# Kernel tuning notes

Measured on AMD Instinct MI355X. Metric: run time of the kernel, lower is better.

## Reference

```python
import jax, jax.numpy as jnp
import numpy as np

IN_DIM = 128
OUT_DIM = 128
HEADS = 4
HEAD_DIM = OUT_DIM // HEADS
N_NODES = 50000
N_EDGES = 800000
NEG_SLOPE = 0.2
LN_EPS = 1e-5


def setup_inputs() -> dict:
    key = jax.random.key(0)
    ks = jax.random.split(key, 10)
    x = jax.random.normal(ks[0], (N_NODES, IN_DIM), dtype=jnp.float32)
    edge_index = jax.random.randint(ks[1], (2, N_EDGES), 0, N_NODES, dtype=jnp.int64)
    s = 1.0 / np.sqrt(IN_DIM)
    W_l = jax.random.normal(ks[2], (IN_DIM, HEADS * HEAD_DIM), dtype=jnp.float32) * s
    b_l = jnp.zeros((HEADS * HEAD_DIM,), dtype=jnp.float32)
    W_r = jax.random.normal(ks[3], (IN_DIM, HEADS * HEAD_DIM), dtype=jnp.float32) * s
    b_r = jnp.zeros((HEADS * HEAD_DIM,), dtype=jnp.float32)
    att = jax.random.normal(ks[4], (HEADS, HEAD_DIM), dtype=jnp.float32) * (1.0 / np.sqrt(HEAD_DIM))
    bias = jnp.zeros((HEADS * HEAD_DIM,), dtype=jnp.float32)
    gamma = jnp.ones((OUT_DIM,), dtype=jnp.float32)
    beta = jnp.zeros((OUT_DIM,), dtype=jnp.float32)
    return {"x": x, "edge_index": edge_index, "W_l": W_l, "b_l": b_l,
            "W_r": W_r, "b_r": b_r, "att": att, "bias": bias,
            "gamma": gamma, "beta": beta}


def reference(x, edge_index, W_l, b_l, W_r, b_r, att, bias, gamma, beta):
    N = x.shape[0]
    src, dst = edge_index[0], edge_index[1]
    # GATv2: separate linear transforms for source and target nodes
    xl = (x @ W_l + b_l).reshape(N, HEADS, HEAD_DIM)  # source / message features
    xr = (x @ W_r + b_r).reshape(N, HEADS, HEAD_DIM)  # target features
    # per-edge attention logits: a^T . leaky_relu(xl[src] + xr[dst])  -> [E, H]
    h = jax.nn.leaky_relu(xl[src] + xr[dst], NEG_SLOPE)
    e = jnp.einsum('ehd,hd->eh', h, att)
    # segment softmax over edges grouped by destination node
    m = jax.ops.segment_max(e, dst, num_segments=N)
    m = jnp.where(jnp.isfinite(m), m, 0.0)  # guard empty segments
    ex = jnp.exp(e - m[dst])
    denom = jax.ops.segment_sum(ex, dst, num_segments=N)
    alpha = ex / (denom[dst] + 1e-16)  # [E, H]
    # scatter-add weighted source features (dropout omitted: eval mode)
    out = jax.ops.segment_sum(alpha[:, :, None] * xl[src], dst, num_segments=N)
    out = out.reshape(N, HEADS * HEAD_DIM) + bias
    # residual (in_dim == out_dim) + LayerNorm
    out = out + x
    mu = out.mean(axis=-1, keepdims=True)
    var = ((out - mu) ** 2).mean(axis=-1, keepdims=True)
    return (out - mu) * jax.lax.rsqrt(var + LN_EPS) * gamma + beta
```

## Files before the change

kernel.cpp:

```cpp
#include <hip/hip_runtime.h>
#include <math.h>

#define NEG_SLOPE 0.2f
#define LN_EPS 1e-5f
#define CAP 64
#define HB 4096
#define RUN 56
#define XSTR 136
#define SMEM_BYTES (64 * XSTR * 2)

typedef __attribute__((ext_vector_type(8))) short s8v;
typedef __attribute__((ext_vector_type(8))) unsigned short u8v;
typedef __attribute__((ext_vector_type(4))) float f4v;
typedef _Float16 h2 __attribute__((ext_vector_type(2)));

__device__ inline unsigned short f2bf(float f) {
    unsigned u = __float_as_uint(f);
    return (unsigned short)((u + 0x7FFFu + ((u >> 16) & 1u)) >> 16);
}

__global__ __launch_bounds__(256) void pre_scat_kernel(
    const int* __restrict__ src, const int* __restrict__ dst,
    const float* __restrict__ Wl, const float* __restrict__ Wr,
    unsigned short* __restrict__ packL, unsigned short* __restrict__ packR,
    unsigned* __restrict__ part, int* __restrict__ cntmat,
    int E, int NBKT) {
    const int bid = blockIdx.x, tid = threadIdx.x;
    if (bid < 2) {
        const float* W = bid ? Wr : Wl;
        unsigned short* pk = bid ? packR : packL;
        #pragma unroll
        for (int it = 0; it < 16; ++it) {
            int pos4 = tid + it * 256;
            int k = pos4 >> 5, c4 = pos4 & 31;
            float4 v = *(const float4*)&W[k * 128 + c4 * 4];
            int t = k >> 5, lane_hi = (k & 31) >> 3, j = k & 7;
            float vv[4] = {v.x, v.y, v.z, v.w};
            #pragma unroll
            for (int u = 0; u < 4; ++u) {
                int n = c4 * 4 + u;
                int idx = ((((n >> 4) * 4 + t) * 64) + lane_hi * 16 + (n & 15)) * 8 + j;
                pk[idx] = f2bf(vv[u]);
            }
        }
        return;
    }
    __shared__ int cnt[256];
    const int sb = bid - 2;
    const int e0 = sb * HB;
    cnt[tid] = 0;
    __syncthreads();
    for (int j = tid; j < HB; j += 256) {
        int e = e0 + j;
        if (e < E) {
            int d = dst[e];
            int b = d >> 8;
            int r = atomicAdd(&cnt[b], 1);
            if (r < RUN)
                part[((size_t)sb * NBKT + b) * RUN + r] =
                    ((unsigned)(d & 255) << 16) | (unsigned)src[e];
        }
    }
    __syncthreads();
    if (tid < NBKT) {
        int c = cnt[tid]; if (c > RUN) c = RUN;
        cntmat[(size_t)sb * NBKT + tid] = c;
    }
}

__global__ __launch_bounds__(256, 4) void fill_tf_kernel(
    const unsigned* __restrict__ part, const int* __restrict__ cntmat,
    unsigned short* __restrict__ csr, int* __restrict__ deg,
    const float* __restrict__ x,
    const unsigned short* __restrict__ packL, const unsigned short* __restrict__ packR,
    const float* __restrict__ bl, const float* __restrict__ br,
    _Float16* __restrict__ xl, _Float16* __restrict__ xr,
    int N, int NBKT, int NSC) {
    const int bid = blockIdx.x, tid = threadIdx.x;
    __shared__ __align__(16) char smem[SMEM_BYTES];

    if (bid < NBKT) {
        int* cur = (int*)smem;
        cur[tid] = 0;
        __syncthreads();
        const int b = bid;
        if (tid < NSC) {
            int cnt = cntmat[(size_t)tid * NBKT + b];
            const unsigned* seg = part + ((size_t)tid * NBKT + b) * RUN;
            for (int i = 0; i < cnt; ++i) {
                unsigned rec = seg[i];
                int dl = rec >> 16;
                int pos = atomicAdd(&cur[dl], 1);
                if (pos < CAP)
                    csr[(size_t)(b * 256 + dl) * CAP + (((pos & 3) << 4) | (pos >> 2))] =
                        (unsigned short)(rec & 0xFFFFu);
            }
        }
        __syncthreads();
        int node = b * 256 + tid;
        if (node < N) deg[node] = cur[tid];
        return;
    }

    unsigned short* xs = (unsigned short*)smem;
    const int tb = bid - NBKT;
    const int blk0 = tb * 64;

    #pragma unroll
    for (int it = 0; it < 8; ++it) {
        int slot = tid + it * 256;
        int row = slot >> 5, c4 = slot & 31;
        int node = blk0 + row;
        float4 v = make_float4(0.f, 0.f, 0.f, 0.f);
        if (node < N) v = *(const float4*)&x[(size_t)node * 128 + 4 * c4];
        ushort4 o;
        o.x = f2bf(v.x); o.y = f2bf(v.y); o.z = f2bf(v.z); o.w = f2bf(v.w);
        *(ushort4*)&xs[row * XSTR + 4 * c4] = o;
    }
    __syncthreads();

    const int wv = tid >> 6, lane = tid & 63;
    const int row = lane & 15, q = lane >> 4;
    const int node0 = blk0 + wv * 16;

    s8v afrag[4];
    #pragma unroll
    for (int t = 0; t < 4; ++t)
        afrag[t] = *(const s8v*)&xs[(wv * 16 + row) * XSTR + t * 32 + q * 8];

    #pragma unroll 1
    for (int side = 0; side < 2; ++side) {
        const unsigned short* __restrict__ pk = side ? packR : packL;
        const float* __restrict__ bb = side ? br : bl;
        _Float16* __restrict__ dsth = side ? xr : xl;

        f4v acc[8];
        #pragma unroll
        for (int nt = 0; nt < 8; ++nt) acc[nt] = (f4v){0.f, 0.f, 0.f, 0.f};

        #pragma unroll
        for (int t = 0; t < 4; ++t) {
            #pragma unroll
            for (int np = 0; np < 2; ++np) {
                s8v bfr[4];
                #pragma unroll
                for (int u = 0; u < 4; ++u)
                    bfr[u] = *(const s8v*)&pk[(((np * 4 + u) * 4 + t) * 64 + lane) * 8];
                #pragma unroll
                for (int u = 0; u < 4; ++u)
                    acc[np * 4 + u] = __builtin_amdgcn_mfma_f32_16x16x32_bf16(
                        afrag[t], bfr[u], acc[np * 4 + u], 0, 0, 0);
            }
        }

        #pragma unroll
        for (int nt = 0; nt < 8; ++nt) {
            float bcol = bb[nt * 16 + row];
            #pragma unroll
            for (int r2 = 0; r2 < 4; ++r2) {
                int nd = node0 + q * 4 + r2;
                if (nd < N)
                    dsth[(size_t)nd * 128 + nt * 16 + row] = (_Float16)(acc[nt][r2] + bcol);
            }
        }
    }
}

__device__ inline void edge_body(float4 raw, const h2* xr2, const h2* av2,
                                 h2 ns2, float& den, float* acc) {
    h2 c[4];
    c[0] = __builtin_bit_cast(h2, raw.x);
    c[1] = __builtin_bit_cast(h2, raw.y);
    c[2] = __builtin_bit_cast(h2, raw.z);
    c[3] = __builtin_bit_cast(h2, raw.w);
    float p = 0.f;
    #pragma unroll
    for (int j = 0; j < 4; ++j) {
        h2 t = c[j] + xr2[j];
        h2 hh = __builtin_elementwise_max(t, t * ns2);
#if __has_builtin(__builtin_amdgcn_fdot2)
        p = __builtin_amdgcn_fdot2(hh, av2[j], p, false);
#else
        p = fmaf((float)hh.x, (float)av2[j].x, p);
        p = fmaf((float)hh.y, (float)av2[j].y, p);
#endif
    }
    p += __shfl_xor(p, 1);
    p += __shfl_xor(p, 2);
    float w = __expf(p);
    den += w;
    #pragma unroll
    for (int j = 0; j < 4; ++j) {
        acc[2 * j]     = fmaf(w, (float)c[j].x, acc[2 * j]);
        acc[2 * j + 1] = fmaf(w, (float)c[j].y, acc[2 * j + 1]);
    }
}

__global__ __launch_bounds__(256) void gat_kernel(
    const int* __restrict__ deg_arr, const unsigned short* __restrict__ csr,
    const _Float16* __restrict__ xl, const _Float16* __restrict__ xr,
    const float* __restrict__ att, const float* __restrict__ x,
    const float* __restrict__ bias, const float* __restrict__ gamma,
    const float* __restrict__ beta, float* __restrict__ out, int N) {
    const int node = blockIdx.x * 4 + (threadIdx.x >> 6);
    const int lane = threadIdx.x & 63;
    if (node >= N) return;
    const int sub = lane & 15;
    const int eg  = lane >> 4;
    const int f0  = sub * 8;

    int dg = deg_arr[node]; if (dg > CAP) dg = CAP;
    const unsigned short* crow = csr + (size_t)node * CAP;
    u8v cidx = *(const u8v*)&crow[eg * 16];

    h2 xr2[4], av2[4];
    {
        float4 xrw = *(const float4*)&xr[(size_t)node * 128 + f0];
        float fw[4]; fw[0] = xrw.x; fw[1] = xrw.y; fw[2] = xrw.z; fw[3] = xrw.w;
        #pragma unroll
        for (int j = 0; j < 4; ++j) xr2[j] = __builtin_bit_cast(h2, fw[j]);
        float4 c0 = *(const float4*)&att[f0];
        float4 c1 = *(const float4*)&att[f0 + 4];
        av2[0] = (h2){(_Float16)c0.x, (_Float16)c0.y};
        av2[1] = (h2){(_Float16)c0.z, (_Float16)c0.w};
        av2[2] = (h2){(_Float16)c1.x, (_Float16)c1.y};
        av2[3] = (h2){(_Float16)c1.z, (_Float16)c1.w};
    }
    const h2 ns2 = (h2){(_Float16)NEG_SLOPE, (_Float16)NEG_SLOPE};

    float4 bufv[8];
    #pragma unroll
    for (int k = 0; k < 8; ++k) {
        int i = eg + 4 * k;
        if (i < dg) bufv[k] = *(const float4*)&xl[(size_t)(unsigned short)cidx[k] * 128 + f0];
    }

    float den0 = 0.f, den1 = 0.f;
    float a0[8] = {0,0,0,0,0,0,0,0}, a1[8] = {0,0,0,0,0,0,0,0};

    #pragma unroll
    for (int k = 0; k < 8; k += 2) {
        if (eg + 4 * k < dg)       edge_body(bufv[k],     xr2, av2, ns2, den0, a0);
        if (eg + 4 * (k + 1) < dg) edge_body(bufv[k + 1], xr2, av2, ns2, den1, a1);
    }

    if (dg > 32) {
        u8v cidx2 = *(const u8v*)&crow[eg * 16 + 8];
        #pragma unroll
        for (int k = 0; k < 8; ++k) {
            int i = eg + 32 + 4 * k;
            if (i < dg) {
                float4 raw = *(const float4*)&xl[(size_t)(unsigned short)cidx2[k] * 128 + f0];
                edge_body(raw, xr2, av2, ns2, (k & 1) ? den1 : den0, (k & 1) ? a1 : a0);
            }
        }
    }

    float den = den0 + den1;
    float acc[8];
    #pragma unroll
    for (int j = 0; j < 8; ++j) acc[j] = a0[j] + a1[j];

    den += __shfl_xor(den, 16); den += __shfl_xor(den, 32);
    #pragma unroll
    for (int j = 0; j < 8; ++j) {
        acc[j] += __shfl_xor(acc[j], 16);
        acc[j] += __shfl_xor(acc[j], 32);
    }

    const float inv = 1.0f / (den + 1e-16f);
    float v[8];
    {
        float4 b0 = *(const float4*)&bias[f0];
        float4 b1 = *(const float4*)&bias[f0 + 4];
        float4 r0 = *(const float4*)&x[(size_t)node * 128 + f0];
        float4 r1 = *(const float4*)&x[(size_t)node * 128 + f0 + 4];
        const float bbf[8] = {b0.x, b0.y, b0.z, b0.w, b1.x, b1.y, b1.z, b1.w};
        const float rrf[8] = {r0.x, r0.y, r0.z, r0.w, r1.x, r1.y, r1.z, r1.w};
        #pragma unroll
        for (int j = 0; j < 8; ++j) v[j] = acc[j] * inv + bbf[j] + rrf[j];
    }

    float s = v[0] + v[1] + v[2] + v[3] + v[4] + v[5] + v[6] + v[7];
    s += __shfl_xor(s, 1); s += __shfl_xor(s, 2);
    s += __shfl_xor(s, 4); s += __shfl_xor(s, 8);
    const float mu = s * (1.0f / 128.0f);

    float d[8], vs = 0.f;
    #pragma unroll
    for (int j = 0; j < 8; ++j) { d[j] = v[j] - mu; vs = fmaf(d[j], d[j], vs); }
    vs += __shfl_xor(vs, 1); vs += __shfl_xor(vs, 2);
    vs += __shfl_xor(vs, 4); vs += __shfl_xor(vs, 8);
    const float rstd = rsqrtf(vs * (1.0f / 128.0f) + LN_EPS);

    if (eg == 0) {
        float4 g0 = *(const float4*)&gamma[f0];
        float4 g1 = *(const float4*)&gamma[f0 + 4];
        float4 e0 = *(const float4*)&beta[f0];
        float4 e1 = *(const float4*)&beta[f0 + 4];
        float4 o0, o1;
        o0.x = d[0] * rstd * g0.x + e0.x;  o0.y = d[1] * rstd * g0.y + e0.y;
        o0.z = d[2] * rstd * g0.z + e0.z;  o0.w = d[3] * rstd * g0.w + e0.w;
        o1.x = d[4] * rstd * g1.x + e1.x;  o1.y = d[5] * rstd * g1.y + e1.y;
        o1.z = d[6] * rstd * g1.z + e1.z;  o1.w = d[7] * rstd * g1.w + e1.w;
        *(float4*)&out[(size_t)node * 128 + f0]     = o0;
        *(float4*)&out[(size_t)node * 128 + f0 + 4] = o1;
    }
}

extern "C" void kernel_launch(void* const* d_in, const int* in_sizes, int n_in,
                              void* d_out, int out_size, void* d_ws, size_t ws_size,
                              hipStream_t stream) {
    const float* x     = (const float*)d_in[0];
    const int*   ei    = (const int*)d_in[1];
    const float* Wl    = (const float*)d_in[2];
    const float* bl    = (const float*)d_in[3];
    const float* Wr    = (const float*)d_in[4];
    const float* br    = (const float*)d_in[5];
    const float* att   = (const float*)d_in[6];
    const float* bias  = (const float*)d_in[7];
    const float* gamma = (const float*)d_in[8];
    const float* beta  = (const float*)d_in[9];

    const int N = in_sizes[0] / 128;
    const int E = in_sizes[1] / 2;
    const int* src = ei;
    const int* dst = ei + E;

    const int NBKT = (N + 255) >> 8;
    const int NSC  = (E + HB - 1) / HB;
    const int TBS  = (N + 63) / 64;

    char* w = (char*)d_ws;
    _Float16*       xl    = (_Float16*)w;        w += (size_t)N * 128 * sizeof(_Float16);
    _Float16*       xr    = (_Float16*)w;        w += (size_t)N * 128 * sizeof(_Float16);
    unsigned short* packL = (unsigned short*)w;  w += 16384 * sizeof(unsigned short);
    unsigned short* packR = (unsigned short*)w;  w += 16384 * sizeof(unsigned short);
    unsigned*       part  = (unsigned*)w;        w += (size_t)NSC * NBKT * RUN * sizeof(unsigned);
    int*            cntmat= (int*)w;             w += (size_t)NSC * NBKT * sizeof(int);
    unsigned short* csr   = (unsigned short*)w;  w += (size_t)N * CAP * sizeof(unsigned short);
    int*            deg   = (int*)w;             w += (size_t)N * sizeof(int);

    pre_scat_kernel<<<2 + NSC, 256, 0, stream>>>(
        src, dst, Wl, Wr, packL, packR, part, cntmat, E, NBKT);
    fill_tf_kernel<<<NBKT + TBS, 256, 0, stream>>>(
        part, cntmat, csr, deg, x, packL, packR, bl, br, xl, xr, N, NBKT, NSC);
    gat_kernel<<<(N + 3) / 4, 256, 0, stream>>>(
        deg, csr, xl, xr, att, x, bias, gamma, beta, (float*)d_out, N);
}
```

Baseline: 163.9 us.

## Pad CSR rows, use wave-uniform edge loop, stage GEMM stores via LDS

The CSR fill step now pads each node's neighbor list up to a multiple of 4 with the node's own index, so the GAT kernel can issue gathers with a wave-uniform trip count (readfirstlane) and mask invalid edges by zeroing their weight instead of using per-lane branches. The gathers are also hoisted ahead of the xr/att loads to start memory traffic sooner. The transform GEMM writes its outputs to shared memory first and then emits coalesced 16-byte stores instead of scattered 2-byte stores. The GAT kernel now launches 1024-thread blocks of 16 nodes, which could change occupancy and scheduling.

```diff
diff --git a/kernel.cpp b/kernel.cpp
--- a/kernel.cpp
+++ b/kernel.cpp
@@ -98,7 +98,13 @@
         }
         __syncthreads();
         int node = b * 256 + tid;
-        if (node < N) deg[node] = cur[tid];
+        if (node < N) {
+            int dgc = cur[tid]; if (dgc > CAP) dgc = CAP;
+            deg[node] = dgc;
+            int dgp = (dgc + 3) & ~3; if (dgp > CAP) dgp = CAP;
+            for (int p = dgc; p < dgp; ++p)
+                csr[(size_t)node * CAP + (((p & 3) << 4) | (p >> 2))] = (unsigned short)node;
+        }
         return;
     }
 
@@ -121,12 +127,14 @@
 
     const int wv = tid >> 6, lane = tid & 63;
     const int row = lane & 15, q = lane >> 4;
-    const int node0 = blk0 + wv * 16;
 
     s8v afrag[4];
     #pragma unroll
     for (int t = 0; t < 4; ++t)
         afrag[t] = *(const s8v*)&xs[(wv * 16 + row) * XSTR + t * 32 + q * 8];
+
+    __syncthreads();
+    _Float16* ys = (_Float16*)smem;
 
     #pragma unroll 1
     for (int side = 0; side < 2; ++side) {
@@ -157,17 +165,26 @@
         for (int nt = 0; nt < 8; ++nt) {
             float bcol = bb[nt * 16 + row];
             #pragma unroll
-            for (int r2 = 0; r2 < 4; ++r2) {
-                int nd = node0 + q * 4 + r2;
-                if (nd < N)
-                    dsth[(size_t)nd * 128 + nt * 16 + row] = (_Float16)(acc[nt][r2] + bcol);
-            }
-        }
+            for (int r2 = 0; r2 < 4; ++r2)
+                ys[(wv * 16 + q * 4 + r2) * XSTR + nt * 16 + row] =
+                    (_Float16)(acc[nt][r2] + bcol);
+        }
+        __syncthreads();
+        #pragma unroll
+        for (int it = 0; it < 4; ++it) {
+            int slot = tid + it * 256;
+            int rrow = slot >> 4, c8 = slot & 15;
+            int nd = blk0 + rrow;
+            if (nd < N)
+                *(float4*)&dsth[(size_t)nd * 128 + c8 * 8] =
+                    *(const float4*)&ys[rrow * XSTR + c8 * 8];
+        }
+        __syncthreads();
     }
 }
 
 __device__ inline void edge_body(float4 raw, const h2* xr2, const h2* av2,
-                                 h2 ns2, float& den, float* acc) {
+                                 h2 ns2, bool valid, float& den, float* acc) {
     h2 c[4];
     c[0] = __builtin_bit_cast(h2, raw.x);
     c[1] = __builtin_bit_cast(h2, raw.y);
@@ -188,6 +205,7 @@
     p += __shfl_xor(p, 1);
     p += __shfl_xor(p, 2);
     float w = __expf(p);
+    w = valid ? w : 0.f;
     den += w;
     #pragma unroll
     for (int j = 0; j < 4; ++j) {
@@ -196,13 +214,13 @@
     }
 }
 
-__global__ __launch_bounds__(256) void gat_kernel(
+__global__ __launch_bounds__(1024) void gat_kernel(
     const int* __restrict__ deg_arr, const unsigned short* __restrict__ csr,
     const _Float16* __restrict__ xl, const _Float16* __restrict__ xr,
     const float* __restrict__ att, const float* __restrict__ x,
     const float* __restrict__ bias, const float* __restrict__ gamma,
     const float* __restrict__ beta, float* __restrict__ out, int N) {
-    const int node = blockIdx.x * 4 + (threadIdx.x >> 6);
+    const int node = blockIdx.x * 16 + (threadIdx.x >> 6);
     const int lane = threadIdx.x & 63;
     if (node >= N) return;
     const int sub = lane & 15;
@@ -210,8 +228,16 @@
     const int f0  = sub * 8;
 
     int dg = deg_arr[node]; if (dg > CAP) dg = CAP;
+    int kmax = (dg + 3) >> 2; if (kmax > 8) kmax = 8;
+    kmax = __builtin_amdgcn_readfirstlane(kmax);
+
     const unsigned short* crow = csr + (size_t)node * CAP;
     u8v cidx = *(const u8v*)&crow[eg * 16];
+
+    float4 bufv[8];
+    #pragma unroll
+    for (int k = 0; k < 8; ++k)
+        if (k < kmax) bufv[k] = *(const float4*)&xl[(size_t)(unsigned short)cidx[k] * 128 + f0];
 
     h2 xr2[4], av2[4];
     {
@@ -228,20 +254,13 @@
     }
     const h2 ns2 = (h2){(_Float16)NEG_SLOPE, (_Float16)NEG_SLOPE};
 
-    float4 bufv[8];
-    #pragma unroll
-    for (int k = 0; k < 8; ++k) {
-        int i = eg + 4 * k;
-        if (i < dg) bufv[k] = *(const float4*)&xl[(size_t)(unsigned short)cidx[k] * 128 + f0];
-    }
-
     float den0 = 0.f, den1 = 0.f;
     float a0[8] = {0,0,0,0,0,0,0,0}, a1[8] = {0,0,0,0,0,0,0,0};
 
     #pragma unroll
     for (int k = 0; k < 8; k += 2) {
-        if (eg + 4 * k < dg)       edge_body(bufv[k],     xr2, av2, ns2, den0, a0);
-        if (eg + 4 * (k + 1) < dg) edge_body(bufv[k + 1], xr2, av2, ns2, den1, a1);
+        if (k < kmax)     edge_body(bufv[k],     xr2, av2, ns2, eg + 4 * k < dg, den0, a0);
+        if (k + 1 < kmax) edge_body(bufv[k + 1], xr2, av2, ns2, eg + 4 * (k + 1) < dg, den1, a1);
     }
 
     if (dg > 32) {
@@ -251,7 +270,7 @@
             int i = eg + 32 + 4 * k;
             if (i < dg) {
                 float4 raw = *(const float4*)&xl[(size_t)(unsigned short)cidx2[k] * 128 + f0];
-                edge_body(raw, xr2, av2, ns2, (k & 1) ? den1 : den0, (k & 1) ? a1 : a0);
+                edge_body(raw, xr2, av2, ns2, true, (k & 1) ? den1 : den0, (k & 1) ? a1 : a0);
             }
         }
     }
@@ -345,6 +364,6 @@
         src, dst, Wl, Wr, packL, packR, part, cntmat, E, NBKT);
     fill_tf_kernel<<<NBKT + TBS, 256, 0, stream>>>(
         part, cntmat, csr, deg, x, packL, packR, bl, br, xl, xr, N, NBKT, NSC);
-    gat_kernel<<<(N + 3) / 4, 256, 0, stream>>>(
+    gat_kernel<<<(N + 15) / 16, 1024, 0, stream>>>(
         deg, csr, xl, xr, att, x, bias, gamma, beta, (float*)d_out, N);
 }
```

After: 186.3 us. 13.6% more time.

## Stage projection output in LDS for coalesced stores; make GAT kernel grid-stride persistent

Applied to the files above, without the earlier changes.

In the projection part of the fused fill/transform kernel, MFMA results are written to shared memory first and then stored to global as 16-byte row-contiguous vectors. This replaces the scattered 2-byte per-lane stores. The gather/attention kernel now launches a fixed grid of 2048 blocks, and each wave loops over nodes with a stride, instead of one wave per node. This cuts launch overhead and keeps per-wave setup (attention vector) resident, but adds extra barriers and reuses the LDS region that held the x tile.

```diff
diff --git a/kernel.cpp b/kernel.cpp
--- a/kernel.cpp
+++ b/kernel.cpp
@@ -121,12 +121,14 @@
 
     const int wv = tid >> 6, lane = tid & 63;
     const int row = lane & 15, q = lane >> 4;
-    const int node0 = blk0 + wv * 16;
 
     s8v afrag[4];
     #pragma unroll
     for (int t = 0; t < 4; ++t)
         afrag[t] = *(const s8v*)&xs[(wv * 16 + row) * XSTR + t * 32 + q * 8];
+
+    __syncthreads();
+    _Float16* ys = (_Float16*)smem;
 
     #pragma unroll 1
     for (int side = 0; side < 2; ++side) {
@@ -157,12 +159,21 @@
         for (int nt = 0; nt < 8; ++nt) {
             float bcol = bb[nt * 16 + row];
             #pragma unroll
-            for (int r2 = 0; r2 < 4; ++r2) {
-                int nd = node0 + q * 4 + r2;
-                if (nd < N)
-                    dsth[(size_t)nd * 128 + nt * 16 + row] = (_Float16)(acc[nt][r2] + bcol);
-            }
-        }
+            for (int r2 = 0; r2 < 4; ++r2)
+                ys[(wv * 16 + q * 4 + r2) * XSTR + nt * 16 + row] =
+                    (_Float16)(acc[nt][r2] + bcol);
+        }
+        __syncthreads();
+        #pragma unroll
+        for (int it = 0; it < 4; ++it) {
+            int slot = tid + it * 256;
+            int rrow = slot >> 4, c8 = slot & 15;
+            int nd = blk0 + rrow;
+            if (nd < N)
+                *(float4*)&dsth[(size_t)nd * 128 + c8 * 8] =
+                    *(const float4*)&ys[rrow * XSTR + c8 * 8];
+        }
+        __syncthreads();
     }
 }
 
@@ -201,24 +212,16 @@
     const _Float16* __restrict__ xl, const _Float16* __restrict__ xr,
     const float* __restrict__ att, const float* __restrict__ x,
     const float* __restrict__ bias, const float* __restrict__ gamma,
-    const float* __restrict__ beta, float* __restrict__ out, int N) {
-    const int node = blockIdx.x * 4 + (threadIdx.x >> 6);
+    const float* __restrict__ beta, float* __restrict__ out,
+    int N, int NWAVES) {
     const int lane = threadIdx.x & 63;
-    if (node >= N) return;
+    const int gw = blockIdx.x * 4 + (threadIdx.x >> 6);
     const int sub = lane & 15;
     const int eg  = lane >> 4;
     const int f0  = sub * 8;
 
-    int dg = deg_arr[node]; if (dg > CAP) dg = CAP;
-    const unsigned short* crow = csr + (size_t)node * CAP;
-    u8v cidx = *(const u8v*)&crow[eg * 16];
-
-    h2 xr2[4], av2[4];
+    h2 av2[4];
     {
-        float4 xrw = *(const float4*)&xr[(size_t)node * 128 + f0];
-        float fw[4]; fw[0] = xrw.x; fw[1] = xrw.y; fw[2] = xrw.z; fw[3] = xrw.w;
-        #pragma unroll
-        for (int j = 0; j < 4; ++j) xr2[j] = __builtin_bit_cast(h2, fw[j]);
         float4 c0 = *(const float4*)&att[f0];
         float4 c1 = *(const float4*)&att[f0 + 4];
         av2[0] = (h2){(_Float16)c0.x, (_Float16)c0.y};
@@ -228,83 +231,97 @@
     }
     const h2 ns2 = (h2){(_Float16)NEG_SLOPE, (_Float16)NEG_SLOPE};
 
-    float4 bufv[8];
-    #pragma unroll
-    for (int k = 0; k < 8; ++k) {
-        int i = eg + 4 * k;
-        if (i < dg) bufv[k] = *(const float4*)&xl[(size_t)(unsigned short)cidx[k] * 128 + f0];
-    }
-
-    float den0 = 0.f, den1 = 0.f;
-    float a0[8] = {0,0,0,0,0,0,0,0}, a1[8] = {0,0,0,0,0,0,0,0};
-
-    #pragma unroll
-    for (int k = 0; k < 8; k += 2) {
-        if (eg + 4 * k < dg)       edge_body(bufv[k],     xr2, av2, ns2, den0, a0);
-        if (eg + 4 * (k + 1) < dg) edge_body(bufv[k + 1], xr2, av2, ns2, den1, a1);
-    }
-
-    if (dg > 32) {
-        u8v cidx2 = *(const u8v*)&crow[eg * 16 + 8];
+    for (int node = gw; node < N; node += NWAVES) {
+        int dg = deg_arr[node]; if (dg > CAP) dg = CAP;
+        const unsigned short* crow = csr + (size_t)node * CAP;
+        u8v cidx = *(const u8v*)&crow[eg * 16];
+
+        h2 xr2[4];
+        {
+            float4 xrw = *(const float4*)&xr[(size_t)node * 128 + f0];
+            float fw[4]; fw[0] = xrw.x; fw[1] = xrw.y; fw[2] = xrw.z; fw[3] = xrw.w;
+            #pragma unroll
+            for (int j = 0; j < 4; ++j) xr2[j] = __builtin_bit_cast(h2, fw[j]);
+        }
+
+        float4 bufv[8];
         #pragma unroll
         for (int k = 0; k < 8; ++k) {
-            int i = eg + 32 + 4 * k;
-            if (i < dg) {
-                float4 raw = *(const float4*)&xl[(size_t)(unsigned short)cidx2[k] * 128 + f0];
-                edge_body(raw, xr2, av2, ns2, (k & 1) ? den1 : den0, (k & 1) ? a1 : a0);
+            int i = eg + 4 * k;
+            if (i < dg) bufv[k] = *(const float4*)&xl[(size_t)(unsigned short)cidx[k] * 128 + f0];
+        }
+
+        float den0 = 0.f, den1 = 0.f;
+        float a0[8] = {0,0,0,0,0,0,0,0}, a1[8] = {0,0,0,0,0,0,0,0};
+
+        #pragma unroll
+        for (int k = 0; k < 8; k += 2) {
+            if (eg + 4 * k < dg)       edge_body(bufv[k],     xr2, av2, ns2, den0, a0);
+            if (eg + 4 * (k + 1) < dg) edge_body(bufv[k + 1], xr2, av2, ns2, den1, a1);
+        }
+
+        if (dg > 32) {
+            u8v cidx2 = *(const u8v*)&crow[eg * 16 + 8];
+            #pragma unroll
+            for (int k = 0; k < 8; ++k) {
+                int i = eg + 32 + 4 * k;
+                if (i < dg) {
+                    float4 raw = *(const float4*)&xl[(size_t)(unsigned short)cidx2[k] * 128 + f0];
+                    edge_body(raw, xr2, av2, ns2, (k & 1) ? den1 : den0, (k & 1) ? a1 : a0);
+                }
             }
         }
-    }
-
-    float den = den0 + den1;
-    float acc[8];
-    #pragma unroll
-    for (int j = 0; j < 8; ++j) acc[j] = a0[j] + a1[j];
-
-    den += __shfl_xor(den, 16); den += __shfl_xor(den, 32);
-    #pragma unroll
-    for (int j = 0; j < 8; ++j) {
-        acc[j] += __shfl_xor(acc[j], 16);
-        acc[j] += __shfl_xor(acc[j], 32);
-    }
-
-    const float inv = 1.0f / (den + 1e-16f);
-    float v[8];
-    {
-        float4 b0 = *(const float4*)&bias[f0];
-        float4 b1 = *(const float4*)&bias[f0 + 4];
-        float4 r0 = *(const float4*)&x[(size_t)node * 128 + f0];
-        float4 r1 = *(const float4*)&x[(size_t)node * 128 + f0 + 4];
-        const float bbf[8] = {b0.x, b0.y, b0.z, b0.w, b1.x, b1.y, b1.z, b1.w};
-        const float rrf[8] = {r0.x, r0.y, r0.z, r0.w, r1.x, r1.y, r1.z, r1.w};
-        #pragma unroll
-        for (int j = 0; j < 8; ++j) v[j] = acc[j] * inv + bbf[j] + rrf[j];
-    }
-
-    float s = v[0] + v[1] + v[2] + v[3] + v[4] + v[5] + v[6] + v[7];
-    s += __shfl_xor(s, 1); s += __shfl_xor(s, 2);
-    s += __shfl_xor(s, 4); s += __shfl_xor(s, 8);
-    const float mu = s * (1.0f / 128.0f);
-
-    float d[8], vs = 0.f;
-    #pragma unroll
-    for (int j = 0; j < 8; ++j) { d[j] = v[j] - mu; vs = fmaf(d[j], d[j], vs); }
-    vs += __shfl_xor(vs, 1); vs += __shfl_xor(vs, 2);
-    vs += __shfl_xor(vs, 4); vs += __shfl_xor(vs, 8);
-    const float rstd = rsqrtf(vs * (1.0f / 128.0f) + LN_EPS);
-
-    if (eg == 0) {
-        float4 g0 = *(const float4*)&gamma[f0];
-        float4 g1 = *(const float4*)&gamma[f0 + 4];
-        float4 e0 = *(const float4*)&beta[f0];
-        float4 e1 = *(const float4*)&beta[f0 + 4];
-        float4 o0, o1;
-        o0.x = d[0] * rstd * g0.x + e0.x;  o0.y = d[1] * rstd * g0.y + e0.y;
-        o0.z = d[2] * rstd * g0.z + e0.z;  o0.w = d[3] * rstd * g0.w + e0.w;
-        o1.x = d[4] * rstd * g1.x + e1.x;  o1.y = d[5] * rstd * g1.y + e1.y;
-        o1.z = d[6] * rstd * g1.z + e1.z;  o1.w = d[7] * rstd * g1.w + e1.w;
-        *(float4*)&out[(size_t)node * 128 + f0]     = o0;
-        *(float4*)&out[(size_t)node * 128 + f0 + 4] = o1;
+
+        float den = den0 + den1;
+        float acc[8];
+        #pragma unroll
+        for (int j = 0; j < 8; ++j) acc[j] = a0[j] + a1[j];
+
+        den += __shfl_xor(den, 16); den += __shfl_xor(den, 32);
+        #pragma unroll
+        for (int j = 0; j < 8; ++j) {
+            acc[j] += __shfl_xor(acc[j], 16);
+            acc[j] += __shfl_xor(acc[j], 32);
+        }
+
+        const float inv = 1.0f / (den + 1e-16f);
+        float v[8];
+        {
+            float4 b0 = *(const float4*)&bias[f0];
+            float4 b1 = *(const float4*)&bias[f0 + 4];
+            float4 r0 = *(const float4*)&x[(size_t)node * 128 + f0];
+            float4 r1 = *(const float4*)&x[(size_t)node * 128 + f0 + 4];
+            const float bbf[8] = {b0.x, b0.y, b0.z, b0.w, b1.x, b1.y, b1.z, b1.w};
+            const float rrf[8] = {r0.x, r0.y, r0.z, r0.w, r1.x, r1.y, r1.z, r1.w};
+            #pragma unroll
+            for (int j = 0; j < 8; ++j) v[j] = acc[j] * inv + bbf[j] + rrf[j];
+        }
+
+        float s = v[0] + v[1] + v[2] + v[3] + v[4] + v[5] + v[6] + v[7];
+        s += __shfl_xor(s, 1); s += __shfl_xor(s, 2);
+        s += __shfl_xor(s, 4); s += __shfl_xor(s, 8);
+        const float mu = s * (1.0f / 128.0f);
+
+        float d[8], vs = 0.f;
+        #pragma unroll
+        for (int j = 0; j < 8; ++j) { d[j] = v[j] - mu; vs = fmaf(d[j], d[j], vs); }
+        vs += __shfl_xor(vs, 1); vs += __shfl_xor(vs, 2);
+        vs += __shfl_xor(vs, 4); vs += __shfl_xor(vs, 8);
+        const float rstd = rsqrtf(vs * (1.0f / 128.0f) + LN_EPS);
+
+        if (eg == 0) {
+            float4 g0 = *(const float4*)&gamma[f0];
+            float4 g1 = *(const float4*)&gamma[f0 + 4];
+            float4 e0 = *(const float4*)&beta[f0];
+            float4 e1 = *(const float4*)&beta[f0 + 4];
+            float4 o0, o1;
+            o0.x = d[0] * rstd * g0.x + e0.x;  o0.y = d[1] * rstd * g0.y + e0.y;
+            o0.z = d[2] * rstd * g0.z + e0.z;  o0.w = d[3] * rstd * g0.w + e0.w;
+            o1.x = d[4] * rstd * g1.x + e1.x;  o1.y = d[5] * rstd * g1.y + e1.y;
+            o1.z = d[6] * rstd * g1.z + e1.z;  o1.w = d[7] * rstd * g1.w + e1.w;
+            *(float4*)&out[(size_t)node * 128 + f0]     = o0;
+            *(float4*)&out[(size_t)node * 128 + f0 + 4] = o1;
+        }
     }
 }
 
@@ -330,6 +347,8 @@
     const int NBKT = (N + 255) >> 8;
     const int NSC  = (E + HB - 1) / HB;
     const int TBS  = (N + 63) / 64;
+    const int GATB = 2048;
+    const int NWAVES = GATB * 4;
 
     char* w = (char*)d_ws;
     _Float16*       xl    = (_Float16*)w;        w += (size_t)N * 128 * sizeof(_Float16);
@@ -345,6 +364,6 @@
         src, dst, Wl, Wr, packL, packR, part, cntmat, E, NBKT);
     fill_tf_kernel<<<NBKT + TBS, 256, 0, stream>>>(
         part, cntmat, csr, deg, x, packL, packR, bl, br, xl, xr, N, NBKT, NSC);
-    gat_kernel<<<(N + 3) / 4, 256, 0, stream>>>(
-        deg, csr, xl, xr, att, x, bias, gamma, beta, (float*)d_out, N);
-}
+    gat_kernel<<<GATB, 256, 0, stream>>>(
+        deg, csr, xl, xr, att, x, bias, gamma, beta, (float*)d_out, N, NWAVES);
+}
```

Measured after the change: 170.4 us. +3.9%, slower.
